# Optimization experiments

Measured on AMD Instinct MI355X. Metric: run time of the kernel, lower is better.

The kernel has to match this reference:

```python
import jax, jax.numpy as jnp
import numpy as np

EMBED = 50
SEQ = 100
NLABEL = 15
HID = 20
VOCAB = 50000
BATCH = 8192


def gru_scan(xs, W, U, b, return_sequences):
    """Keras GRUCell (reset_after=True, gate order z,r,h).
    xs: (B, T, D). W: (D, 3H), U: (H, 3H), b: (2, 3H) [input bias, recurrent bias].
    """
    B = xs.shape[0]
    H = U.shape[0]
    bi, br = b[0], b[1]
    h0 = jnp.zeros((B, H), dtype=xs.dtype)

    def step(h, x_t):
        mx = x_t @ W + bi                      # (B, 3H)
        mh = h @ U + br                        # (B, 3H)
        xz, xr, xh = mx[:, :H], mx[:, H:2*H], mx[:, 2*H:]
        hz, hr, hh_ = mh[:, :H], mh[:, H:2*H], mh[:, 2*H:]
        z = jax.nn.sigmoid(xz + hz)
        r = jax.nn.sigmoid(xr + hr)
        hh = jnp.tanh(xh + r * hh_)
        h_new = z * h + (1.0 - z) * hh
        return h_new, h_new

    xs_t = jnp.swapaxes(xs, 0, 1)              # (T, B, D)
    h_last, hs = jax.lax.scan(step, h0, xs_t)
    if return_sequences:
        return jnp.swapaxes(hs, 0, 1)          # (B, T, H)
    return h_last                               # (B, H)


def setup_inputs() -> dict:
    key = jax.random.key(0)
    ks = jax.random.split(key, 9)
    s = 0.05
    return {
        "x": jax.random.randint(ks[0], (BATCH, SEQ), 0, VOCAB),
        "emb_table": jax.random.normal(ks[1], (VOCAB, EMBED), jnp.float32) * s,
        "W1": jax.random.normal(ks[2], (EMBED, 3 * HID), jnp.float32) * s,
        "U1": jax.random.normal(ks[3], (HID, 3 * HID), jnp.float32) * s,
        "b1": jnp.zeros((2, 3 * HID), jnp.float32),
        "W2": jax.random.normal(ks[4], (HID, 3 * HID), jnp.float32) * s,
        "U2": jax.random.normal(ks[5], (HID, 3 * HID), jnp.float32) * s,
        "b2": jnp.zeros((2, 3 * HID), jnp.float32),
        "Wd": jax.random.normal(ks[6], (HID, NLABEL), jnp.float32) * s,
        "bd": jnp.zeros((NLABEL,), jnp.float32),
        "drop_rate": 0,
    }


def reference(x, emb_table, W1, U1, b1, W2, U2, b2, Wd, bd, drop_rate):
    emb = emb_table[x]                               # (B, T, E)
    seq = gru_scan(emb, W1, U1, b1, return_sequences=True)   # (B, T, H)
    enc = gru_scan(seq, W2, U2, b2, return_sequences=False)  # (B, H)
    # drop_rate == 0 -> tf.nn.dropout is identity
    logits = enc @ Wd + bd                           # (B, 15)
    return logits
```

## Files before the change

kernel.cpp:

```cpp
#include <hip/hip_runtime.h>
#include <hip/hip_bf16.h>
#include <hip/hip_fp16.h>

#define SEQ_T 100
#define HID 20
#define EMB_D 50
#define VOCAB_N 50000
#define TABW 60
#define NTILE 3125
#define BBLK 782

typedef short sh8 __attribute__((ext_vector_type(8)));
typedef float f4  __attribute__((ext_vector_type(4)));

#define OFF_U1P 0
#define OFF_W2P 600
#define OFF_U2P 1200
#define OFF_B1  3600
#define OFF_B2  3720
#define OFF_WD  3840
#define OFF_BD  4140
#define OFF_TAB 4160

__device__ __forceinline__ float ldf(const void* p, int i, int isf) {
  return isf ? ((const float*)p)[i]
             : __bfloat162float(((const __hip_bfloat16*)p)[i]);
}
__device__ __forceinline__ short f2bf(float f) {
  unsigned u = __float_as_uint(f);
  u += 0x7fffu + ((u >> 16) & 1u);
  return (short)(u >> 16);
}
__device__ __forceinline__ float rdl(float v, int l) {
  return __uint_as_float(__builtin_amdgcn_readlane(__float_as_uint(v), l));
}
__device__ __forceinline__ int detect_isf(const void* emb) {
  uint4 dv = ((const uint4*)emb)[threadIdx.x & 63];
  int big = 0;
#pragma unroll
  for (int i = 0; i < 4; ++i) {
    unsigned w = ((const unsigned*)&dv)[i];
    big |= (((w >> 7) & 0xFF) >= 140) | (((w >> 23) & 0xFF) >= 140);
  }
  return (__ballot(big) != 0ull) ? 1 : 0;
}

__global__ __launch_bounds__(256) void build_table(
    const void* __restrict__ emb, const void* __restrict__ W1,
    const void* __restrict__ b1,
    const void* __restrict__ U1, const void* __restrict__ W2,
    const void* __restrict__ U2, const void* __restrict__ b2,
    const void* __restrict__ Wd, const void* __restrict__ bd,
    float* __restrict__ ws)
{
  const int isf = detect_isf(emb);
  if (blockIdx.x == 0) {
    const int t = threadIdx.x;
    unsigned* wsu = (unsigned*)ws;
    for (int i = t; i < 600; i += 256) {
      const int j = i / 10, p = i % 10;
      const int k0 = 2 * p, k1 = 2 * p + 1;
#define PK(M) ((unsigned)__half_as_ushort(__float2half_rn(ldf(M, k0 * 60 + j, isf))) | \
               ((unsigned)__half_as_ushort(__float2half_rn(ldf(M, k1 * 60 + j, isf))) << 16))
      wsu[OFF_U1P + i] = PK(U1);
      wsu[OFF_W2P + i] = PK(W2);
      wsu[OFF_U2P + i] = PK(U2);
#undef PK
    }
    for (int i = t; i < 120; i += 256) {
      ws[OFF_B1 + i] = ldf(b1, i, isf);
      ws[OFF_B2 + i] = ldf(b2, i, isf);
    }
    for (int i = t; i < 300; i += 256) ws[OFF_WD + i] = ldf(Wd, i, isf);
    for (int i = t; i < 15;  i += 256) ws[OFF_BD + i] = ldf(bd, i, isf);
  }

  const int L = threadIdx.x & 63, q = L >> 4, c = L & 15;
  const int wid = blockIdx.x * 4 + (threadIdx.x >> 6);
  float* __restrict__ tab = ws + OFF_TAB;

  __shared__ int4 sB[64][8];
  if (threadIdx.x < 64) {
#pragma unroll
    for (int nt = 0; nt < 4; ++nt) {
      const int col = nt * 16 + c;
      sh8 B0, B1;
#pragma unroll
      for (int jj = 0; jj < 8; ++jj) {
        const int k0 = q * 8 + jj, k1 = 32 + q * 8 + jj;
        B0[jj] = (col < TABW) ? f2bf(ldf(W1, k0 * TABW + col, isf)) : (short)0;
        B1[jj] = (col < TABW && k1 < EMB_D)
                     ? f2bf(ldf(W1, k1 * TABW + col, isf)) : (short)0;
      }
      sB[L][nt * 2]     = *(const int4*)&B0;
      sB[L][nt * 2 + 1] = *(const int4*)&B1;
    }
  }
  float bi[4];
#pragma unroll
  for (int nt = 0; nt < 4; ++nt) {
    const int col = nt * 16 + c;
    bi[nt] = (col < TABW) ? ldf(b1, col, isf) : 0.f;
  }
  __syncthreads();

  for (int tile = wid; tile < NTILE; tile += BBLK * 4) {
    const int v0 = tile * 16;
    sh8 A0, A1;
#pragma unroll
    for (int jj = 0; jj < 8; ++jj) { A0[jj] = 0; A1[jj] = 0; }
    if (!isf) {
      const unsigned short* eb = (const unsigned short*)emb;
      const size_t rb = (size_t)(v0 + c) * EMB_D;
#pragma unroll
      for (int i = 0; i < 4; ++i) {
        unsigned d = *(const unsigned*)(eb + rb + q * 8 + 2 * i);
        A0[2 * i] = (short)(d & 0xffff); A0[2 * i + 1] = (short)(d >> 16);
      }
      const int k1b = 32 + q * 8;
#pragma unroll
      for (int i = 0; i < 4; ++i) {
        const int k = k1b + 2 * i;
        if (k + 1 < EMB_D) {
          unsigned d = *(const unsigned*)(eb + rb + k);
          A1[2 * i] = (short)(d & 0xffff); A1[2 * i + 1] = (short)(d >> 16);
        }
      }
    } else {
      const float* ef = (const float*)emb;
      const size_t rb = (size_t)(v0 + c) * EMB_D;
#pragma unroll
      for (int jj = 0; jj < 8; ++jj) {
        const int k0 = q * 8 + jj, k1 = 32 + q * 8 + jj;
        A0[jj] = f2bf(ef[rb + k0]);
        A1[jj] = (k1 < EMB_D) ? f2bf(ef[rb + k1]) : (short)0;
      }
    }
#pragma unroll
    for (int nt = 0; nt < 4; ++nt) {
      int4 b0i = sB[L][nt * 2], b1i = sB[L][nt * 2 + 1];
      sh8 B0 = *(const sh8*)&b0i, B1 = *(const sh8*)&b1i;
      const int col = nt * 16 + c;
      f4 acc = { bi[nt], bi[nt], bi[nt], bi[nt] };
      acc = __builtin_amdgcn_mfma_f32_16x16x32_bf16(A0, B0, acc, 0, 0, 0);
      acc = __builtin_amdgcn_mfma_f32_16x16x32_bf16(A1, B1, acc, 0, 0, 0);
      if (col < TABW) {
#pragma unroll
        for (int r = 0; r < 4; ++r)
          tab[(size_t)(v0 + q * 4 + r) * TABW + col] = acc[r];
      }
    }
  }
}

__global__ __launch_bounds__(256, 8) void gru_main(
    const int* __restrict__ x, const float* __restrict__ ws,
    const void* __restrict__ emb, void* __restrict__ out)
{
  const int isf = detect_isf(emb);
  const int j = threadIdx.x & 63;
  const int e = __builtin_amdgcn_readfirstlane(blockIdx.x * 4 + (threadIdx.x >> 6));
  const int jc = j < TABW ? j : 0;

  const int* xr = x + (size_t)e * SEQ_T;
  const float* tab = ws + OFF_TAB;
  const int o1 = jc * 40;
  const int jc4 = jc * 4;
  const int a1 = ((j - 20) & 63) * 4;
  const int a2 = ((j + 40) & 63) * 4;
  const float br1 = ws[OFF_B1 + 60 + jc];
  const float bi2 = ws[OFF_B2 + jc];
  const float br2 = ws[OFF_B2 + 60 + jc];
  float h2out;

  asm volatile(
    "global_load_dwordx4 v[10:13], %[o1], %[wsp] offset:0\n\t"
    "global_load_dwordx4 v[14:17], %[o1], %[wsp] offset:16\n\t"
    "global_load_dwordx2 v[18:19], %[o1], %[wsp] offset:32\n\t"
    "v_add_u32 v44, 0x960, %[o1]\n\t"
    "v_add_u32 v45, 0x12c0, %[o1]\n\t"
    "global_load_dwordx4 v[20:23], v44, %[wsp] offset:0\n\t"
    "global_load_dwordx4 v[24:27], v44, %[wsp] offset:16\n\t"
    "global_load_dwordx2 v[28:29], v44, %[wsp] offset:32\n\t"
    "global_load_dwordx4 v[30:33], v45, %[wsp] offset:0\n\t"
    "global_load_dwordx4 v[34:37], v45, %[wsp] offset:16\n\t"
    "global_load_dwordx2 v[38:39], v45, %[wsp] offset:32\n\t"
    "s_mov_b64 s[20:21], 0\n\ts_mov_b64 s[22:23], 0\n\t"
    "s_mov_b64 s[24:25], 0\n\ts_mov_b64 s[26:27], 0\n\t"
    "s_mov_b64 s[28:29], 0\n\t"
    "s_mov_b64 s[30:31], 0\n\ts_mov_b64 s[32:33], 0\n\t"
    "s_mov_b64 s[34:35], 0\n\ts_mov_b64 s[36:37], 0\n\t"
    "s_mov_b64 s[38:39], 0\n\t"
    "v_mov_b32 v40, 0\n\t"
    "v_mov_b32 v41, 0\n\t"
    "s_load_dword s65, %[xp], 0x0\n\t"
    "s_load_dword s66, %[xp], 0x4\n\t"
    "s_waitcnt lgkmcnt(0)\n\t"
    "s_mul_i32 s65, s65, 240\n\t"
    "s_mul_i32 s66, s66, 240\n\t"
    "v_add_u32 v50, s65, %[jc4]\n\t"
    "global_load_dword v42, v50, %[tabp]\n\t"
    "v_add_u32 v50, s66, %[jc4]\n\t"
    "global_load_dword v43, v50, %[tabp]\n\t"
    "s_load_dword s65, %[xp], 0x8\n\t"
    "s_movk_i32 s64, 0xc\n\t"
    "s_movk_i32 s67, 0x64\n\t"
    "s_waitcnt vmcnt(0)\n\t"
    "0:\n\t"
    "v_mov_b32 v44, %[br1]\n\t"
    "v_dot2_f32_f16 v44, s20, v10, v44\n\t"
    "v_dot2_f32_f16 v44, s21, v11, v44\n\t"
    "v_dot2_f32_f16 v44, s22, v12, v44\n\t"
    "v_dot2_f32_f16 v44, s23, v13, v44\n\t"
    "v_dot2_f32_f16 v44, s24, v14, v44\n\t"
    "v_dot2_f32_f16 v44, s25, v15, v44\n\t"
    "v_dot2_f32_f16 v44, s26, v16, v44\n\t"
    "v_dot2_f32_f16 v44, s27, v17, v44\n\t"
    "v_dot2_f32_f16 v44, s28, v18, v44\n\t"
    "v_dot2_f32_f16 v44, s29, v19, v44\n\t"
    "v_add_f32 v45, v42, v44\n\t"
    "v_mul_f32 v45, 0xbfb8aa3b, v45\n\t"
    "v_exp_f32 v45, v45\n\t"
    "s_nop 1\n\t"
    "v_add_f32 v45, 1.0, v45\n\t"
    "v_rcp_f32 v45, v45\n\t"
    "s_nop 1\n\t"
    "ds_bpermute_b32 v46, %[a1], v45\n\t"
    "s_waitcnt lgkmcnt(0)\n\t"
    "v_fma_f32 v47, v46, v44, v42\n\t"
    "v_mul_f32 v47, 0x4038aa3b, v47\n\t"
    "v_exp_f32 v47, v47\n\t"
    "s_nop 1\n\t"
    "v_add_f32 v47, 1.0, v47\n\t"
    "v_rcp_f32 v47, v47\n\t"
    "s_nop 1\n\t"
    "v_fma_f32 v47, -2.0, v47, 1.0\n\t"
    "ds_bpermute_b32 v46, %[a2], v47\n\t"
    "s_waitcnt lgkmcnt(0)\n\t"
    "v_sub_f32 v48, v40, v46\n\t"
    "v_fma_f32 v40, v45, v48, v46\n\t"
    "s_nop 1\n\t"
    "v_cvt_f16_f32 v46, v40\n\t"
    "s_nop 1\n\t"
    "ds_swizzle_b32 v47, v46 offset:0x041F\n\t"
    "s_waitcnt lgkmcnt(0)\n\t"
    "v_pack_b32_f16 v46, v46, v47\n\t"
    "s_nop 1\n\t"
    "v_readlane_b32 s20, v46, 0\n\t"
    "v_readlane_b32 s21, v46, 2\n\t"
    "v_readlane_b32 s22, v46, 4\n\t"
    "v_readlane_b32 s23, v46, 6\n\t"
    "v_readlane_b32 s24, v46, 8\n\t"
    "v_readlane_b32 s25, v46, 10\n\t"
    "v_readlane_b32 s26, v46, 12\n\t"
    "v_readlane_b32 s27, v46, 14\n\t"
    "v_readlane_b32 s28, v46, 16\n\t"
    "v_readlane_b32 s29, v46, 18\n\t"
    "s_mul_i32 s66, s65, 240\n\t"
    "v_add_u32 v50, s66, %[jc4]\n\t"
    "s_waitcnt vmcnt(0)\n\t"
    "v_mov_b32 v42, v43\n\t"
    "global_load_dword v43, v50, %[tabp]\n\t"
    "s_min_u32 s64, s64, 396\n\t"
    "s_load_dword s65, %[xp], s64\n\t"
    "s_add_u32 s64, s64, 4\n\t"
    "v_mov_b32 v44, %[bi2]\n\t"
    "v_mov_b32 v48, %[br2]\n\t"
    "v_dot2_f32_f16 v44, s20, v20, v44\n\t"
    "v_dot2_f32_f16 v48, s30, v30, v48\n\t"
    "v_dot2_f32_f16 v44, s21, v21, v44\n\t"
    "v_dot2_f32_f16 v48, s31, v31, v48\n\t"
    "v_dot2_f32_f16 v44, s22, v22, v44\n\t"
    "v_dot2_f32_f16 v48, s32, v32, v48\n\t"
    "v_dot2_f32_f16 v44, s23, v23, v44\n\t"
    "v_dot2_f32_f16 v48, s33, v33, v48\n\t"
    "v_dot2_f32_f16 v44, s24, v24, v44\n\t"
    "v_dot2_f32_f16 v48, s34, v34, v48\n\t"
    "v_dot2_f32_f16 v44, s25, v25, v44\n\t"
    "v_dot2_f32_f16 v48, s35, v35, v48\n\t"
    "v_dot2_f32_f16 v44, s26, v26, v44\n\t"
    "v_dot2_f32_f16 v48, s36, v36, v48\n\t"
    "v_dot2_f32_f16 v44, s27, v27, v44\n\t"
    "v_dot2_f32_f16 v48, s37, v37, v48\n\t"
    "v_dot2_f32_f16 v44, s28, v28, v44\n\t"
    "v_dot2_f32_f16 v48, s38, v38, v48\n\t"
    "v_dot2_f32_f16 v44, s29, v29, v44\n\t"
    "v_dot2_f32_f16 v48, s39, v39, v48\n\t"
    "v_add_f32 v45, v44, v48\n\t"
    "v_mul_f32 v45, 0xbfb8aa3b, v45\n\t"
    "v_exp_f32 v45, v45\n\t"
    "s_nop 1\n\t"
    "v_add_f32 v45, 1.0, v45\n\t"
    "v_rcp_f32 v45, v45\n\t"
    "s_nop 1\n\t"
    "ds_bpermute_b32 v46, %[a1], v45\n\t"
    "s_waitcnt lgkmcnt(0)\n\t"
    "v_fma_f32 v47, v46, v48, v44\n\t"
    "v_mul_f32 v47, 0x4038aa3b, v47\n\t"
    "v_exp_f32 v47, v47\n\t"
    "s_nop 1\n\t"
    "v_add_f32 v47, 1.0, v47\n\t"
    "v_rcp_f32 v47, v47\n\t"
    "s_nop 1\n\t"
    "v_fma_f32 v47, -2.0, v47, 1.0\n\t"
    "ds_bpermute_b32 v46, %[a2], v47\n\t"
    "s_waitcnt lgkmcnt(0)\n\t"
    "v_sub_f32 v49, v41, v46\n\t"
    "v_fma_f32 v41, v45, v49, v46\n\t"
    "s_nop 1\n\t"
    "v_cvt_f16_f32 v46, v41\n\t"
    "s_nop 1\n\t"
    "ds_swizzle_b32 v47, v46 offset:0x041F\n\t"
    "s_waitcnt lgkmcnt(0)\n\t"
    "v_pack_b32_f16 v46, v46, v47\n\t"
    "s_nop 1\n\t"
    "v_readlane_b32 s30, v46, 0\n\t"
    "v_readlane_b32 s31, v46, 2\n\t"
    "v_readlane_b32 s32, v46, 4\n\t"
    "v_readlane_b32 s33, v46, 6\n\t"
    "v_readlane_b32 s34, v46, 8\n\t"
    "v_readlane_b32 s35, v46, 10\n\t"
    "v_readlane_b32 s36, v46, 12\n\t"
    "v_readlane_b32 s37, v46, 14\n\t"
    "v_readlane_b32 s38, v46, 16\n\t"
    "v_readlane_b32 s39, v46, 18\n\t"
    "s_sub_u32 s67, s67, 1\n\t"
    "s_cmp_lg_u32 s67, 0\n\t"
    "s_cbranch_scc1 0b\n\t"
    "s_waitcnt vmcnt(0) lgkmcnt(0)\n\t"
    "v_mov_b32 %[h2o], v41\n\t"
    : [h2o] "=v"(h2out)
    : [wsp] "s"(ws), [xp] "s"(xr), [tabp] "s"(tab),
      [o1] "v"(o1), [jc4] "v"(jc4), [a1] "v"(a1), [a2] "v"(a2),
      [br1] "v"(br1), [bi2] "v"(bi2), [br2] "v"(br2)
    : "memory", "vcc", "scc",
      "v10","v11","v12","v13","v14","v15","v16","v17","v18","v19",
      "v20","v21","v22","v23","v24","v25","v26","v27","v28","v29",
      "v30","v31","v32","v33","v34","v35","v36","v37","v38","v39",
      "v40","v41","v42","v43","v44","v45","v46","v47","v48","v49","v50",
      "s20","s21","s22","s23","s24","s25","s26","s27","s28","s29",
      "s30","s31","s32","s33","s34","s35","s36","s37","s38","s39",
      "s64","s65","s66","s67");

  if (j < 15) {
    float a = ws[OFF_BD + j];
#pragma unroll
    for (int k = 0; k < HID; ++k)
      a = fmaf(rdl(h2out, k), ws[OFF_WD + k * 15 + j], a);
    if (isf) ((float*)out)[(size_t)e * 15 + j] = a;
    else ((__hip_bfloat16*)out)[(size_t)e * 15 + j] = __float2bfloat16(a);
  }
}

extern "C" void kernel_launch(void* const* d_in, const int* in_sizes, int n_in,
                              void* d_out, int out_size, void* d_ws, size_t ws_size,
                              hipStream_t stream) {
  const int* x    = (const int*)d_in[0];
  const void* emb = d_in[1];
  const void* W1  = d_in[2];
  const void* U1  = d_in[3];
  const void* b1  = d_in[4];
  const void* W2  = d_in[5];
  const void* U2  = d_in[6];
  const void* b2  = d_in[7];
  const void* Wd  = d_in[8];
  const void* bd  = d_in[9];
  float* ws = (float*)d_ws;

  build_table<<<BBLK, 256, 0, stream>>>(
      emb, W1, b1, U1, W2, U2, b2, Wd, bd, ws);
  gru_main<<<2048, 256, 0, stream>>>(x, ws, emb, d_out);
}
```

Before: 240.6 us.

## Interleave two batch rows per wave, wavefront-skew GRU layers, fold exp scales into weights

Each wave now processes two sequences interleaved, so their independent dependency chains can hide each other's latency. Layer 1 and layer 2 are skewed by one timestep and computed in the same iteration. The hidden state is passed through LDS ds_write/ds_read instead of readlane into SGPRs. The log2e sigmoid/tanh scaling constants are folded into the packed weights, biases and the precomputed input table. The table is stored as fp16 instead of fp32 to halve gather traffic. The costs are a much higher VGPR footprint (occupancy hint lowered to 4), half as many blocks, and extra fp16 rounding of the table.

```diff
diff --git a/kernel.cpp b/kernel.cpp
--- a/kernel.cpp
+++ b/kernel.cpp
@@ -43,6 +43,9 @@
     big |= (((w >> 7) & 0xFF) >= 140) | (((w >> 23) & 0xFF) >= 140);
   }
   return (__ballot(big) != 0ull) ? 1 : 0;
+}
+__device__ __forceinline__ float gsc(int col) {
+  return (col < 40) ? -1.44269504f : 2.88539008f;
 }
 
 __global__ __launch_bounds__(256) void build_table(
@@ -60,16 +63,17 @@
     for (int i = t; i < 600; i += 256) {
       const int j = i / 10, p = i % 10;
       const int k0 = 2 * p, k1 = 2 * p + 1;
-#define PK(M) ((unsigned)__half_as_ushort(__float2half_rn(ldf(M, k0 * 60 + j, isf))) | \
-               ((unsigned)__half_as_ushort(__float2half_rn(ldf(M, k1 * 60 + j, isf))) << 16))
+      const float s = gsc(j);
+#define PK(M) ((unsigned)__half_as_ushort(__float2half_rn(ldf(M, k0 * 60 + j, isf) * s)) | \
+               ((unsigned)__half_as_ushort(__float2half_rn(ldf(M, k1 * 60 + j, isf) * s)) << 16))
       wsu[OFF_U1P + i] = PK(U1);
       wsu[OFF_W2P + i] = PK(W2);
       wsu[OFF_U2P + i] = PK(U2);
 #undef PK
     }
     for (int i = t; i < 120; i += 256) {
-      ws[OFF_B1 + i] = ldf(b1, i, isf);
-      ws[OFF_B2 + i] = ldf(b2, i, isf);
+      ws[OFF_B1 + i] = ldf(b1, i, isf) * (i >= 60 ? gsc(i - 60) : 1.f);
+      ws[OFF_B2 + i] = ldf(b2, i, isf) * gsc(i % 60);
     }
     for (int i = t; i < 300; i += 256) ws[OFF_WD + i] = ldf(Wd, i, isf);
     for (int i = t; i < 15;  i += 256) ws[OFF_BD + i] = ldf(bd, i, isf);
@@ -77,7 +81,7 @@
 
   const int L = threadIdx.x & 63, q = L >> 4, c = L & 15;
   const int wid = blockIdx.x * 4 + (threadIdx.x >> 6);
-  float* __restrict__ tab = ws + OFF_TAB;
+  unsigned short* __restrict__ tab16 = (unsigned short*)(ws + OFF_TAB);
 
   __shared__ int4 sB[64][8];
   if (threadIdx.x < 64) {
@@ -145,210 +149,491 @@
       acc = __builtin_amdgcn_mfma_f32_16x16x32_bf16(A0, B0, acc, 0, 0, 0);
       acc = __builtin_amdgcn_mfma_f32_16x16x32_bf16(A1, B1, acc, 0, 0, 0);
       if (col < TABW) {
+        const float s = gsc(col);
 #pragma unroll
         for (int r = 0; r < 4; ++r)
-          tab[(size_t)(v0 + q * 4 + r) * TABW + col] = acc[r];
+          tab16[(size_t)(v0 + q * 4 + r) * TABW + col] =
+              __half_as_ushort(__float2half_rn(acc[r] * s));
       }
     }
   }
 }
 
-__global__ __launch_bounds__(256, 8) void gru_main(
+__global__ __launch_bounds__(256, 4) void gru_main(
     const int* __restrict__ x, const float* __restrict__ ws,
     const void* __restrict__ emb, void* __restrict__ out)
 {
   const int isf = detect_isf(emb);
   const int j = threadIdx.x & 63;
-  const int e = __builtin_amdgcn_readfirstlane(blockIdx.x * 4 + (threadIdx.x >> 6));
+  const int e = __builtin_amdgcn_readfirstlane(blockIdx.x * 8 + (threadIdx.x >> 6) * 2);
   const int jc = j < TABW ? j : 0;
 
   const int* xr = x + (size_t)e * SEQ_T;
-  const float* tab = ws + OFF_TAB;
+  const unsigned short* tab = (const unsigned short*)(ws + OFF_TAB);
   const int o1 = jc * 40;
-  const int jc4 = jc * 4;
+  const int jc2 = jc * 2;
   const int a1 = ((j - 20) & 63) * 4;
   const int a2 = ((j + 40) & 63) * 4;
   const float br1 = ws[OFF_B1 + 60 + jc];
   const float bi2 = ws[OFF_B2 + jc];
   const float br2 = ws[OFF_B2 + 60 + jc];
-  float h2out;
+
+  __shared__ char sbuf[2048];
+  const unsigned lb = (unsigned)(uintptr_t)&sbuf[0] + (threadIdx.x >> 6) * 512;
+  const int lmap = (j < 20 ? 2 * j : 40 + 2 * (j - 20));
+  const int wadA = (int)(lb + lmap),       radA = (int)lb;
+  const int wadB = (int)(lb + 256 + lmap), radB = (int)(lb + 256);
+  float h2oA, h2oB;
 
   asm volatile(
     "global_load_dwordx4 v[10:13], %[o1], %[wsp] offset:0\n\t"
     "global_load_dwordx4 v[14:17], %[o1], %[wsp] offset:16\n\t"
     "global_load_dwordx2 v[18:19], %[o1], %[wsp] offset:32\n\t"
-    "v_add_u32 v44, 0x960, %[o1]\n\t"
-    "v_add_u32 v45, 0x12c0, %[o1]\n\t"
-    "global_load_dwordx4 v[20:23], v44, %[wsp] offset:0\n\t"
-    "global_load_dwordx4 v[24:27], v44, %[wsp] offset:16\n\t"
-    "global_load_dwordx2 v[28:29], v44, %[wsp] offset:32\n\t"
-    "global_load_dwordx4 v[30:33], v45, %[wsp] offset:0\n\t"
-    "global_load_dwordx4 v[34:37], v45, %[wsp] offset:16\n\t"
-    "global_load_dwordx2 v[38:39], v45, %[wsp] offset:32\n\t"
-    "s_mov_b64 s[20:21], 0\n\ts_mov_b64 s[22:23], 0\n\t"
-    "s_mov_b64 s[24:25], 0\n\ts_mov_b64 s[26:27], 0\n\t"
-    "s_mov_b64 s[28:29], 0\n\t"
-    "s_mov_b64 s[30:31], 0\n\ts_mov_b64 s[32:33], 0\n\t"
-    "s_mov_b64 s[34:35], 0\n\ts_mov_b64 s[36:37], 0\n\t"
-    "s_mov_b64 s[38:39], 0\n\t"
-    "v_mov_b32 v40, 0\n\t"
-    "v_mov_b32 v41, 0\n\t"
+    "v_add_u32 v98, 0x960, %[o1]\n\t"
+    "v_add_u32 v109, 0x12c0, %[o1]\n\t"
+    "global_load_dwordx4 v[20:23], v98, %[wsp] offset:0\n\t"
+    "global_load_dwordx4 v[24:27], v98, %[wsp] offset:16\n\t"
+    "global_load_dwordx2 v[28:29], v98, %[wsp] offset:32\n\t"
+    "global_load_dwordx4 v[30:33], v109, %[wsp] offset:0\n\t"
+    "global_load_dwordx4 v[34:37], v109, %[wsp] offset:16\n\t"
+    "global_load_dwordx2 v[38:39], v109, %[wsp] offset:32\n\t"
+    "v_mov_b32 v80, 0\n\tv_mov_b32 v81, 0\n\t"
+    "v_mov_b32 v82, 0\n\tv_mov_b32 v83, 0\n\t"
+    "v_mov_b32 v50, 0\n\tv_mov_b32 v51, 0\n\t"
+    "v_mov_b32 v52, 0\n\tv_mov_b32 v53, 0\n\t"
+    "v_mov_b32 v54, 0\n\tv_mov_b32 v55, 0\n\t"
+    "v_mov_b32 v56, 0\n\tv_mov_b32 v57, 0\n\t"
+    "v_mov_b32 v58, 0\n\tv_mov_b32 v59, 0\n\t"
+    "v_mov_b32 v70, 0\n\tv_mov_b32 v71, 0\n\t"
+    "v_mov_b32 v72, 0\n\tv_mov_b32 v73, 0\n\t"
+    "v_mov_b32 v74, 0\n\tv_mov_b32 v75, 0\n\t"
+    "v_mov_b32 v76, 0\n\tv_mov_b32 v77, 0\n\t"
+    "v_mov_b32 v78, 0\n\tv_mov_b32 v79, 0\n\t"
     "s_load_dword s65, %[xp], 0x0\n\t"
     "s_load_dword s66, %[xp], 0x4\n\t"
-    "s_waitcnt lgkmcnt(0)\n\t"
-    "s_mul_i32 s65, s65, 240\n\t"
-    "s_mul_i32 s66, s66, 240\n\t"
-    "v_add_u32 v50, s65, %[jc4]\n\t"
-    "global_load_dword v42, v50, %[tabp]\n\t"
-    "v_add_u32 v50, s66, %[jc4]\n\t"
-    "global_load_dword v43, v50, %[tabp]\n\t"
-    "s_load_dword s65, %[xp], 0x8\n\t"
-    "s_movk_i32 s64, 0xc\n\t"
-    "s_movk_i32 s67, 0x64\n\t"
-    "s_waitcnt vmcnt(0)\n\t"
+    "s_load_dword s68, %[xp], 0x8\n\t"
+    "s_load_dword s71, %[xp], 0x190\n\t"
+    "s_load_dword s72, %[xp], 0x194\n\t"
+    "s_load_dword s73, %[xp], 0x198\n\t"
+    "s_waitcnt lgkmcnt(0)\n\t"
+    "s_mul_i32 s65, s65, 120\n\t"
+    "s_mul_i32 s66, s66, 120\n\t"
+    "s_mul_i32 s68, s68, 120\n\t"
+    "s_mul_i32 s71, s71, 120\n\t"
+    "s_mul_i32 s72, s72, 120\n\t"
+    "s_mul_i32 s73, s73, 120\n\t"
+    "v_add_u32 v98, s65, %[jc2]\n\t"
+    "global_load_ushort v97, v98, %[tabp]\n\t"
+    "v_add_u32 v98, s71, %[jc2]\n\t"
+    "global_load_ushort v108, v98, %[tabp]\n\t"
+    "v_add_u32 v98, s66, %[jc2]\n\t"
+    "global_load_ushort v84, v98, %[tabp]\n\t"
+    "v_add_u32 v98, s72, %[jc2]\n\t"
+    "global_load_ushort v86, v98, %[tabp]\n\t"
+    "v_add_u32 v98, s68, %[jc2]\n\t"
+    "global_load_ushort v85, v98, %[tabp]\n\t"
+    "v_add_u32 v98, s73, %[jc2]\n\t"
+    "global_load_ushort v87, v98, %[tabp]\n\t"
+    "s_load_dword s65, %[xp], 0xc\n\t"
+    "s_load_dword s68, %[xp], 0x10\n\t"
+    "s_load_dword s71, %[xp], 0x19c\n\t"
+    "s_load_dword s73, %[xp], 0x1a0\n\t"
+    "s_movk_i32 s64, 0x14\n\t"
+    "s_movk_i32 s69, 0x18\n\t"
+    "s_movk_i32 s70, 0x1a4\n\t"
+    "s_movk_i32 s72, 0x1a8\n\t"
+    "s_movk_i32 s67, 0x32\n\t"
+    "s_waitcnt vmcnt(4)\n\t"
+    "v_cvt_f32_f16 v97, v97\n\t"
+    "v_cvt_f32_f16 v108, v108\n\t"
+    "v_mov_b32 v88, %[br1]\n\t"
+    "v_mov_b32 v99, %[br1]\n\t"
+    "v_add_f32 v91, v97, v88\n\t"
+    "v_add_f32 v102, v108, v99\n\t"
+    "v_exp_f32 v91, v91\n\t"
+    "v_exp_f32 v102, v102\n\t"
+    "s_nop 1\n\t"
+    "v_add_f32 v91, 1.0, v91\n\t"
+    "v_add_f32 v102, 1.0, v102\n\t"
+    "v_rcp_f32 v91, v91\n\t"
+    "v_rcp_f32 v102, v102\n\t"
+    "s_nop 1\n\t"
+    "ds_bpermute_b32 v93, %[a1], v91\n\t"
+    "ds_bpermute_b32 v104, %[a1], v102\n\t"
+    "s_waitcnt lgkmcnt(0)\n\t"
+    "v_fma_f32 v95, v93, v88, v97\n\t"
+    "v_fma_f32 v106, v104, v99, v108\n\t"
+    "v_exp_f32 v95, v95\n\t"
+    "v_exp_f32 v106, v106\n\t"
+    "s_nop 1\n\t"
+    "v_add_f32 v95, 1.0, v95\n\t"
+    "v_add_f32 v106, 1.0, v106\n\t"
+    "v_rcp_f32 v95, v95\n\t"
+    "v_rcp_f32 v106, v106\n\t"
+    "s_nop 1\n\t"
+    "v_fma_f32 v95, -2.0, v95, 1.0\n\t"
+    "v_fma_f32 v106, -2.0, v106, 1.0\n\t"
+    "ds_bpermute_b32 v93, %[a2], v95\n\t"
+    "ds_bpermute_b32 v104, %[a2], v106\n\t"
+    "s_waitcnt lgkmcnt(0)\n\t"
+    "v_sub_f32 v97, v80, v93\n\t"
+    "v_fma_f32 v80, v91, v97, v93\n\t"
+    "v_sub_f32 v108, v82, v104\n\t"
+    "v_fma_f32 v82, v102, v108, v104\n\t"
+    "v_cvt_f16_f32 v93, v80\n\t"
+    "v_cvt_f16_f32 v104, v82\n\t"
+    "s_nop 1\n\t"
+    "ds_write_b16 %[wadA], v93\n\t"
+    "ds_write_b16 %[wadB], v104\n\t"
+    "ds_read_b128 v[40:43], %[radA]\n\t"
+    "ds_read_b128 v[44:47], %[radA] offset:16\n\t"
+    "ds_read_b64  v[48:49], %[radA] offset:32\n\t"
+    "ds_read_b128 v[60:63], %[radB]\n\t"
+    "ds_read_b128 v[64:67], %[radB] offset:16\n\t"
+    "ds_read_b64  v[68:69], %[radB] offset:32\n\t"
     "0:\n\t"
-    "v_mov_b32 v44, %[br1]\n\t"
-    "v_dot2_f32_f16 v44, s20, v10, v44\n\t"
-    "v_dot2_f32_f16 v44, s21, v11, v44\n\t"
-    "v_dot2_f32_f16 v44, s22, v12, v44\n\t"
-    "v_dot2_f32_f16 v44, s23, v13, v44\n\t"
-    "v_dot2_f32_f16 v44, s24, v14, v44\n\t"
-    "v_dot2_f32_f16 v44, s25, v15, v44\n\t"
-    "v_dot2_f32_f16 v44, s26, v16, v44\n\t"
-    "v_dot2_f32_f16 v44, s27, v17, v44\n\t"
-    "v_dot2_f32_f16 v44, s28, v18, v44\n\t"
-    "v_dot2_f32_f16 v44, s29, v19, v44\n\t"
-    "v_add_f32 v45, v42, v44\n\t"
-    "v_mul_f32 v45, 0xbfb8aa3b, v45\n\t"
-    "v_exp_f32 v45, v45\n\t"
+    "s_waitcnt lgkmcnt(0)\n\t"
+    "v_dot2_f32_f16 v88, v40, v10, %[br1]\n\t"
+    "v_dot2_f32_f16 v89, v40, v20, %[bi2]\n\t"
+    "v_dot2_f32_f16 v90, v50, v30, %[br2]\n\t"
+    "v_dot2_f32_f16 v99, v60, v10, %[br1]\n\t"
+    "v_dot2_f32_f16 v100, v60, v20, %[bi2]\n\t"
+    "v_dot2_f32_f16 v101, v70, v30, %[br2]\n\t"
+    "v_dot2_f32_f16 v88, v41, v11, v88\n\t"
+    "v_dot2_f32_f16 v89, v41, v21, v89\n\t"
+    "v_dot2_f32_f16 v90, v51, v31, v90\n\t"
+    "v_dot2_f32_f16 v99, v61, v11, v99\n\t"
+    "v_dot2_f32_f16 v100, v61, v21, v100\n\t"
+    "v_dot2_f32_f16 v101, v71, v31, v101\n\t"
+    "v_dot2_f32_f16 v88, v42, v12, v88\n\t"
+    "v_dot2_f32_f16 v89, v42, v22, v89\n\t"
+    "v_dot2_f32_f16 v90, v52, v32, v90\n\t"
+    "v_dot2_f32_f16 v99, v62, v12, v99\n\t"
+    "v_dot2_f32_f16 v100, v62, v22, v100\n\t"
+    "v_dot2_f32_f16 v101, v72, v32, v101\n\t"
+    "v_dot2_f32_f16 v88, v43, v13, v88\n\t"
+    "v_dot2_f32_f16 v89, v43, v23, v89\n\t"
+    "v_dot2_f32_f16 v90, v53, v33, v90\n\t"
+    "v_dot2_f32_f16 v99, v63, v13, v99\n\t"
+    "v_dot2_f32_f16 v100, v63, v23, v100\n\t"
+    "v_dot2_f32_f16 v101, v73, v33, v101\n\t"
+    "v_dot2_f32_f16 v88, v44, v14, v88\n\t"
+    "v_dot2_f32_f16 v89, v44, v24, v89\n\t"
+    "v_dot2_f32_f16 v90, v54, v34, v90\n\t"
+    "v_dot2_f32_f16 v99, v64, v14, v99\n\t"
+    "v_dot2_f32_f16 v100, v64, v24, v100\n\t"
+    "v_dot2_f32_f16 v101, v74, v34, v101\n\t"
+    "v_dot2_f32_f16 v88, v45, v15, v88\n\t"
+    "v_dot2_f32_f16 v89, v45, v25, v89\n\t"
+    "v_dot2_f32_f16 v90, v55, v35, v90\n\t"
+    "v_dot2_f32_f16 v99, v65, v15, v99\n\t"
+    "v_dot2_f32_f16 v100, v65, v25, v100\n\t"
+    "v_dot2_f32_f16 v101, v75, v35, v101\n\t"
+    "v_dot2_f32_f16 v88, v46, v16, v88\n\t"
+    "v_dot2_f32_f16 v89, v46, v26, v89\n\t"
+    "v_dot2_f32_f16 v90, v56, v36, v90\n\t"
+    "v_dot2_f32_f16 v99, v66, v16, v99\n\t"
+    "v_dot2_f32_f16 v100, v66, v26, v100\n\t"
+    "v_dot2_f32_f16 v101, v76, v36, v101\n\t"
+    "v_dot2_f32_f16 v88, v47, v17, v88\n\t"
+    "v_dot2_f32_f16 v89, v47, v27, v89\n\t"
+    "v_dot2_f32_f16 v90, v57, v37, v90\n\t"
+    "v_dot2_f32_f16 v99, v67, v17, v99\n\t"
+    "v_dot2_f32_f16 v100, v67, v27, v100\n\t"
+    "v_dot2_f32_f16 v101, v77, v37, v101\n\t"
+    "v_dot2_f32_f16 v88, v48, v18, v88\n\t"
+    "v_dot2_f32_f16 v89, v48, v28, v89\n\t"
+    "v_dot2_f32_f16 v90, v58, v38, v90\n\t"
+    "v_dot2_f32_f16 v99, v68, v18, v99\n\t"
+    "v_dot2_f32_f16 v100, v68, v28, v100\n\t"
+    "v_dot2_f32_f16 v101, v78, v38, v101\n\t"
+    "v_dot2_f32_f16 v88, v49, v19, v88\n\t"
+    "v_dot2_f32_f16 v89, v49, v29, v89\n\t"
+    "v_dot2_f32_f16 v90, v59, v39, v90\n\t"
+    "v_dot2_f32_f16 v99, v69, v19, v99\n\t"
+    "v_dot2_f32_f16 v100, v69, v29, v100\n\t"
+    "v_dot2_f32_f16 v101, v79, v39, v101\n\t"
+    "s_waitcnt vmcnt(2)\n\t"
+    "v_cvt_f32_f16 v84, v84\n\t"
+    "v_cvt_f32_f16 v86, v86\n\t"
     "s_nop 1\n\t"
-    "v_add_f32 v45, 1.0, v45\n\t"
-    "v_rcp_f32 v45, v45\n\t"
+    "v_add_f32 v91, v84, v88\n\t"
+    "v_add_f32 v92, v89, v90\n\t"
+    "v_add_f32 v102, v86, v99\n\t"
+    "v_add_f32 v103, v100, v101\n\t"
+    "v_exp_f32 v91, v91\n\t"
+    "v_exp_f32 v92, v92\n\t"
+    "v_exp_f32 v102, v102\n\t"
+    "v_exp_f32 v103, v103\n\t"
+    "v_add_f32 v91, 1.0, v91\n\t"
+    "v_add_f32 v92, 1.0, v92\n\t"
+    "v_add_f32 v102, 1.0, v102\n\t"
+    "v_add_f32 v103, 1.0, v103\n\t"
+    "v_rcp_f32 v91, v91\n\t"
+    "v_rcp_f32 v92, v92\n\t"
+    "v_rcp_f32 v102, v102\n\t"
+    "v_rcp_f32 v103, v103\n\t"
+    "ds_bpermute_b32 v93, %[a1], v91\n\t"
+    "ds_bpermute_b32 v94, %[a1], v92\n\t"
+    "ds_bpermute_b32 v104, %[a1], v102\n\t"
+    "ds_bpermute_b32 v105, %[a1], v103\n\t"
+    "s_waitcnt lgkmcnt(0)\n\t"
+    "v_fma_f32 v95, v93, v88, v84\n\t"
+    "v_fma_f32 v96, v94, v90, v89\n\t"
+    "v_fma_f32 v106, v104, v99, v86\n\t"
+    "v_fma_f32 v107, v105, v101, v100\n\t"
+    "s_mul_i32 s66, s65, 120\n\t"
+    "v_add_u32 v98, s66, %[jc2]\n\t"
+    "global_load_ushort v84, v98, %[tabp]\n\t"
+    "s_min_u32 s64, s64, 0x18c\n\t"
+    "s_load_dword s65, %[xp], s64\n\t"
+    "s_add_u32 s64, s64, 8\n\t"
+    "s_mul_i32 s66, s71, 120\n\t"
+    "v_add_u32 v109, s66, %[jc2]\n\t"
+    "global_load_ushort v86, v109, %[tabp]\n\t"
+    "s_min_u32 s70, s70, 0x31c\n\t"
+    "s_load_dword s71, %[xp], s70\n\t"
+    "s_add_u32 s70, s70, 8\n\t"
+    "v_exp_f32 v95, v95\n\t"
+    "v_exp_f32 v96, v96\n\t"
+    "v_exp_f32 v106, v106\n\t"
+    "v_exp_f32 v107, v107\n\t"
+    "v_add_f32 v95, 1.0, v95\n\t"
+    "v_add_f32 v96, 1.0, v96\n\t"
+    "v_add_f32 v106, 1.0, v106\n\t"
+    "v_add_f32 v107, 1.0, v107\n\t"
+    "v_rcp_f32 v95, v95\n\t"
+    "v_rcp_f32 v96, v96\n\t"
+    "v_rcp_f32 v106, v106\n\t"
+    "v_rcp_f32 v107, v107\n\t"
+    "v_fma_f32 v95, -2.0, v95, 1.0\n\t"
+    "v_fma_f32 v96, -2.0, v96, 1.0\n\t"
+    "v_fma_f32 v106, -2.0, v106, 1.0\n\t"
+    "v_fma_f32 v107, -2.0, v107, 1.0\n\t"
+    "ds_bpermute_b32 v93, %[a2], v95\n\t"
+    "ds_bpermute_b32 v94, %[a2], v96\n\t"
+    "ds_bpermute_b32 v104, %[a2], v106\n\t"
+    "ds_bpermute_b32 v105, %[a2], v107\n\t"
+    "s_waitcnt lgkmcnt(0)\n\t"
+    "v_sub_f32 v97, v80, v93\n\t"
+    "v_fma_f32 v80, v91, v97, v93\n\t"
+    "v_sub_f32 v97, v81, v94\n\t"
+    "v_fma_f32 v81, v92, v97, v94\n\t"
+    "v_sub_f32 v108, v82, v104\n\t"
+    "v_fma_f32 v82, v102, v108, v104\n\t"
+    "v_sub_f32 v108, v83, v105\n\t"
+    "v_fma_f32 v83, v103, v108, v105\n\t"
+    "v_cvt_f16_f32 v93, v80\n\t"
+    "v_cvt_f16_f32 v94, v81\n\t"
+    "v_cvt_f16_f32 v104, v82\n\t"
+    "v_cvt_f16_f32 v105, v83\n\t"
+    "ds_write_b16 %[wadA], v93\n\t"
+    "ds_write_b16 %[wadA], v94 offset:128\n\t"
+    "ds_write_b16 %[wadB], v104\n\t"
+    "ds_write_b16 %[wadB], v105 offset:128\n\t"
+    "ds_read_b128 v[40:43], %[radA]\n\t"
+    "ds_read_b128 v[44:47], %[radA] offset:16\n\t"
+    "ds_read_b64  v[48:49], %[radA] offset:32\n\t"
+    "ds_read_b128 v[50:53], %[radA] offset:128\n\t"
+    "ds_read_b128 v[54:57], %[radA] offset:144\n\t"
+    "ds_read_b64  v[58:59], %[radA] offset:160\n\t"
+    "ds_read_b128 v[60:63], %[radB]\n\t"
+    "ds_read_b128 v[64:67], %[radB] offset:16\n\t"
+    "ds_read_b64  v[68:69], %[radB] offset:32\n\t"
+    "ds_read_b128 v[70:73], %[radB] offset:128\n\t"
+    "ds_read_b128 v[74:77], %[radB] offset:144\n\t"
+    "ds_read_b64  v[78:79], %[radB] offset:160\n\t"
+    "s_waitcnt lgkmcnt(0)\n\t"
+    "v_dot2_f32_f16 v88, v40, v10, %[br1]\n\t"
+    "v_dot2_f32_f16 v89, v40, v20, %[bi2]\n\t"
+    "v_dot2_f32_f16 v90, v50, v30, %[br2]\n\t"
+    "v_dot2_f32_f16 v99, v60, v10, %[br1]\n\t"
+    "v_dot2_f32_f16 v100, v60, v20, %[bi2]\n\t"
+    "v_dot2_f32_f16 v101, v70, v30, %[br2]\n\t"
+    "v_dot2_f32_f16 v88, v41, v11, v88\n\t"
+    "v_dot2_f32_f16 v89, v41, v21, v89\n\t"
+    "v_dot2_f32_f16 v90, v51, v31, v90\n\t"
+    "v_dot2_f32_f16 v99, v61, v11, v99\n\t"
+    "v_dot2_f32_f16 v100, v61, v21, v100\n\t"
+    "v_dot2_f32_f16 v101, v71, v31, v101\n\t"
+    "v_dot2_f32_f16 v88, v42, v12, v88\n\t"
+    "v_dot2_f32_f16 v89, v42, v22, v89\n\t"
+    "v_dot2_f32_f16 v90, v52, v32, v90\n\t"
+    "v_dot2_f32_f16 v99, v62, v12, v99\n\t"
+    "v_dot2_f32_f16 v100, v62, v22, v100\n\t"
+    "v_dot2_f32_f16 v101, v72, v32, v101\n\t"
+    "v_dot2_f32_f16 v88, v43, v13, v88\n\t"
+    "v_dot2_f32_f16 v89, v43, v23, v89\n\t"
+    "v_dot2_f32_f16 v90, v53, v33, v90\n\t"
+    "v_dot2_f32_f16 v99, v63, v13, v99\n\t"
+    "v_dot2_f32_f16 v100, v63, v23, v100\n\t"
+    "v_dot2_f32_f16 v101, v73, v33, v101\n\t"
+    "v_dot2_f32_f16 v88, v44, v14, v88\n\t"
+    "v_dot2_f32_f16 v89, v44, v24, v89\n\t"
+    "v_dot2_f32_f16 v90, v54, v34, v90\n\t"
+    "v_dot2_f32_f16 v99, v64, v14, v99\n\t"
+    "v_dot2_f32_f16 v100, v64, v24, v100\n\t"
+    "v_dot2_f32_f16 v101, v74, v34, v101\n\t"
+    "v_dot2_f32_f16 v88, v45, v15, v88\n\t"
+    "v_dot2_f32_f16 v89, v45, v25, v89\n\t"
+    "v_dot2_f32_f16 v90, v55, v35, v90\n\t"
+    "v_dot2_f32_f16 v99, v65, v15, v99\n\t"
+    "v_dot2_f32_f16 v100, v65, v25, v100\n\t"
+    "v_dot2_f32_f16 v101, v75, v35, v101\n\t"
+    "v_dot2_f32_f16 v88, v46, v16, v88\n\t"
+    "v_dot2_f32_f16 v89, v46, v26, v89\n\t"
+    "v_dot2_f32_f16 v90, v56, v36, v90\n\t"
+    "v_dot2_f32_f16 v99, v66, v16, v99\n\t"
+    "v_dot2_f32_f16 v100, v66, v26, v100\n\t"
+    "v_dot2_f32_f16 v101, v76, v36, v101\n\t"
+    "v_dot2_f32_f16 v88, v47, v17, v88\n\t"
+    "v_dot2_f32_f16 v89, v47, v27, v89\n\t"
+    "v_dot2_f32_f16 v90, v57, v37, v90\n\t"
+    "v_dot2_f32_f16 v99, v67, v17, v99\n\t"
+    "v_dot2_f32_f16 v100, v67, v27, v100\n\t"
+    "v_dot2_f32_f16 v101, v77, v37, v101\n\t"
+    "v_dot2_f32_f16 v88, v48, v18, v88\n\t"
+    "v_dot2_f32_f16 v89, v48, v28, v89\n\t"
+    "v_dot2_f32_f16 v90, v58, v38, v90\n\t"
+    "v_dot2_f32_f16 v99, v68, v18, v99\n\t"
+    "v_dot2_f32_f16 v100, v68, v28, v100\n\t"
+    "v_dot2_f32_f16 v101, v78, v38, v101\n\t"
+    "v_dot2_f32_f16 v88, v49, v19, v88\n\t"
+    "v_dot2_f32_f16 v89, v49, v29, v89\n\t"
+    "v_dot2_f32_f16 v90, v59, v39, v90\n\t"
+    "v_dot2_f32_f16 v99, v69, v19, v99\n\t"
+    "v_dot2_f32_f16 v100, v69, v29, v100\n\t"
+    "v_dot2_f32_f16 v101, v79, v39, v101\n\t"
+    "s_waitcnt vmcnt(2)\n\t"
+    "v_cvt_f32_f16 v85, v85\n\t"
+    "v_cvt_f32_f16 v87, v87\n\t"
     "s_nop 1\n\t"
-    "ds_bpermute_b32 v46, %[a1], v45\n\t"
-    "s_waitcnt lgkmcnt(0)\n\t"
-    "v_fma_f32 v47, v46, v44, v42\n\t"
-    "v_mul_f32 v47, 0x4038aa3b, v47\n\t"
-    "v_exp_f32 v47, v47\n\t"
-    "s_nop 1\n\t"
-    "v_add_f32 v47, 1.0, v47\n\t"
-    "v_rcp_f32 v47, v47\n\t"
-    "s_nop 1\n\t"
-    "v_fma_f32 v47, -2.0, v47, 1.0\n\t"
-    "ds_bpermute_b32 v46, %[a2], v47\n\t"
-    "s_waitcnt lgkmcnt(0)\n\t"
-    "v_sub_f32 v48, v40, v46\n\t"
-    "v_fma_f32 v40, v45, v48, v46\n\t"
-    "s_nop 1\n\t"
-    "v_cvt_f16_f32 v46, v40\n\t"
-    "s_nop 1\n\t"
-    "ds_swizzle_b32 v47, v46 offset:0x041F\n\t"
-    "s_waitcnt lgkmcnt(0)\n\t"
-    "v_pack_b32_f16 v46, v46, v47\n\t"
-    "s_nop 1\n\t"
-    "v_readlane_b32 s20, v46, 0\n\t"
-    "v_readlane_b32 s21, v46, 2\n\t"
-    "v_readlane_b32 s22, v46, 4\n\t"
-    "v_readlane_b32 s23, v46, 6\n\t"
-    "v_readlane_b32 s24, v46, 8\n\t"
-    "v_readlane_b32 s25, v46, 10\n\t"
-    "v_readlane_b32 s26, v46, 12\n\t"
-    "v_readlane_b32 s27, v46, 14\n\t"
-    "v_readlane_b32 s28, v46, 16\n\t"
-    "v_readlane_b32 s29, v46, 18\n\t"
-    "s_mul_i32 s66, s65, 240\n\t"
-    "v_add_u32 v50, s66, %[jc4]\n\t"
-    "s_waitcnt vmcnt(0)\n\t"
-    "v_mov_b32 v42, v43\n\t"
-    "global_load_dword v43, v50, %[tabp]\n\t"
-    "s_min_u32 s64, s64, 396\n\t"
-    "s_load_dword s65, %[xp], s64\n\t"
-    "s_add_u32 s64, s64, 4\n\t"
-    "v_mov_b32 v44, %[bi2]\n\t"
-    "v_mov_b32 v48, %[br2]\n\t"
-    "v_dot2_f32_f16 v44, s20, v20, v44\n\t"
-    "v_dot2_f32_f16 v48, s30, v30, v48\n\t"
-    "v_dot2_f32_f16 v44, s21, v21, v44\n\t"
-    "v_dot2_f32_f16 v48, s31, v31, v48\n\t"
-    "v_dot2_f32_f16 v44, s22, v22, v44\n\t"
-    "v_dot2_f32_f16 v48, s32, v32, v48\n\t"
-    "v_dot2_f32_f16 v44, s23, v23, v44\n\t"
-    "v_dot2_f32_f16 v48, s33, v33, v48\n\t"
-    "v_dot2_f32_f16 v44, s24, v24, v44\n\t"
-    "v_dot2_f32_f16 v48, s34, v34, v48\n\t"
-    "v_dot2_f32_f16 v44, s25, v25, v44\n\t"
-    "v_dot2_f32_f16 v48, s35, v35, v48\n\t"
-    "v_dot2_f32_f16 v44, s26, v26, v44\n\t"
-    "v_dot2_f32_f16 v48, s36, v36, v48\n\t"
-    "v_dot2_f32_f16 v44, s27, v27, v44\n\t"
-    "v_dot2_f32_f16 v48, s37, v37, v48\n\t"
-    "v_dot2_f32_f16 v44, s28, v28, v44\n\t"
-    "v_dot2_f32_f16 v48, s38, v38, v48\n\t"
-    "v_dot2_f32_f16 v44, s29, v29, v44\n\t"
-    "v_dot2_f32_f16 v48, s39, v39, v48\n\t"
-    "v_add_f32 v45, v44, v48\n\t"
-    "v_mul_f32 v45, 0xbfb8aa3b, v45\n\t"
-    "v_exp_f32 v45, v45\n\t"
-    "s_nop 1\n\t"
-    "v_add_f32 v45, 1.0, v45\n\t"
-    "v_rcp_f32 v45, v45\n\t"
-    "s_nop 1\n\t"
-    "ds_bpermute_b32 v46, %[a1], v45\n\t"
-    "s_waitcnt lgkmcnt(0)\n\t"
-    "v_fma_f32 v47, v46, v48, v44\n\t"
-    "v_mul_f32 v47, 0x4038aa3b, v47\n\t"
-    "v_exp_f32 v47, v47\n\t"
-    "s_nop 1\n\t"
-    "v_add_f32 v47, 1.0, v47\n\t"
-    "v_rcp_f32 v47, v47\n\t"
-    "s_nop 1\n\t"
-    "v_fma_f32 v47, -2.0, v47, 1.0\n\t"
-    "ds_bpermute_b32 v46, %[a2], v47\n\t"
-    "s_waitcnt lgkmcnt(0)\n\t"
-    "v_sub_f32 v49, v41, v46\n\t"
-    "v_fma_f32 v41, v45, v49, v46\n\t"
-    "s_nop 1\n\t"
-    "v_cvt_f16_f32 v46, v41\n\t"
-    "s_nop 1\n\t"
-    "ds_swizzle_b32 v47, v46 offset:0x041F\n\t"
-    "s_waitcnt lgkmcnt(0)\n\t"
-    "v_pack_b32_f16 v46, v46, v47\n\t"
-    "s_nop 1\n\t"
-    "v_readlane_b32 s30, v46, 0\n\t"
-    "v_readlane_b32 s31, v46, 2\n\t"
-    "v_readlane_b32 s32, v46, 4\n\t"
-    "v_readlane_b32 s33, v46, 6\n\t"
-    "v_readlane_b32 s34, v46, 8\n\t"
-    "v_readlane_b32 s35, v46, 10\n\t"
-    "v_readlane_b32 s36, v46, 12\n\t"
-    "v_readlane_b32 s37, v46, 14\n\t"
-    "v_readlane_b32 s38, v46, 16\n\t"
-    "v_readlane_b32 s39, v46, 18\n\t"
+    "v_add_f32 v91, v85, v88\n\t"
+    "v_add_f32 v92, v89, v90\n\t"
+    "v_add_f32 v102, v87, v99\n\t"
+    "v_add_f32 v103, v100, v101\n\t"
+    "v_exp_f32 v91, v91\n\t"
+    "v_exp_f32 v92, v92\n\t"
+    "v_exp_f32 v102, v102\n\t"
+    "v_exp_f32 v103, v103\n\t"
+    "v_add_f32 v91, 1.0, v91\n\t"
+    "v_add_f32 v92, 1.0, v92\n\t"
+    "v_add_f32 v102, 1.0, v102\n\t"
+    "v_add_f32 v103, 1.0, v103\n\t"
+    "v_rcp_f32 v91, v91\n\t"
+    "v_rcp_f32 v92, v92\n\t"
+    "v_rcp_f32 v102, v102\n\t"
+    "v_rcp_f32 v103, v103\n\t"
+    "ds_bpermute_b32 v93, %[a1], v91\n\t"
+    "ds_bpermute_b32 v94, %[a1], v92\n\t"
+    "ds_bpermute_b32 v104, %[a1], v102\n\t"
+    "ds_bpermute_b32 v105, %[a1], v103\n\t"
+    "s_waitcnt lgkmcnt(0)\n\t"
+    "v_fma_f32 v95, v93, v88, v85\n\t"
+    "v_fma_f32 v96, v94, v90, v89\n\t"
+    "v_fma_f32 v106, v104, v99, v87\n\t"
+    "v_fma_f32 v107, v105, v101, v100\n\t"
+    "s_mul_i32 s66, s68, 120\n\t"
+    "v_add_u32 v98, s66, %[jc2]\n\t"
+    "global_load_ushort v85, v98, %[tabp]\n\t"
+    "s_min_u32 s69, s69, 0x188\n\t"
+    "s_load_dword s68, %[xp], s69\n\t"
+    "s_add_u32 s69, s69, 8\n\t"
+    "s_mul_i32 s66, s73, 120\n\t"
+    "v_add_u32 v109, s66, %[jc2]\n\t"
+    "global_load_ushort v87, v109, %[tabp]\n\t"
+    "s_min_u32 s72, s72, 0x318\n\t"
+    "s_load_dword s73, %[xp], s72\n\t"
+    "s_add_u32 s72, s72, 8\n\t"
+    "v_exp_f32 v95, v95\n\t"
+    "v_exp_f32 v96, v96\n\t"
+    "v_exp_f32 v106, v106\n\t"
+    "v_exp_f32 v107, v107\n\t"
+    "v_add_f32 v95, 1.0, v95\n\t"
+    "v_add_f32 v96, 1.0, v96\n\t"
+    "v_add_f32 v106, 1.0, v106\n\t"
+    "v_add_f32 v107, 1.0, v107\n\t"
+    "v_rcp_f32 v95, v95\n\t"
+    "v_rcp_f32 v96, v96\n\t"
+    "v_rcp_f32 v106, v106\n\t"
+    "v_rcp_f32 v107, v107\n\t"
+    "v_fma_f32 v95, -2.0, v95, 1.0\n\t"
+    "v_fma_f32 v96, -2.0, v96, 1.0\n\t"
+    "v_fma_f32 v106, -2.0, v106, 1.0\n\t"
+    "v_fma_f32 v107, -2.0, v107, 1.0\n\t"
+    "ds_bpermute_b32 v93, %[a2], v95\n\t"
+    "ds_bpermute_b32 v94, %[a2], v96\n\t"
+    "ds_bpermute_b32 v104, %[a2], v106\n\t"
+    "ds_bpermute_b32 v105, %[a2], v107\n\t"
+    "s_waitcnt lgkmcnt(0)\n\t"
+    "v_sub_f32 v97, v80, v93\n\t"
+    "v_fma_f32 v80, v91, v97, v93\n\t"
+    "v_sub_f32 v97, v81, v94\n\t"
+    "v_fma_f32 v81, v92, v97, v94\n\t"
+    "v_sub_f32 v108, v82, v104\n\t"
+    "v_fma_f32 v82, v102, v108, v104\n\t"
+    "v_sub_f32 v108, v83, v105\n\t"
+    "v_fma_f32 v83, v103, v108, v105\n\t"
+    "v_cvt_f16_f32 v93, v80\n\t"
+    "v_cvt_f16_f32 v94, v81\n\t"
+    "v_cvt_f16_f32 v104, v82\n\t"
+    "v_cvt_f16_f32 v105, v83\n\t"
+    "ds_write_b16 %[wadA], v93\n\t"
+    "ds_write_b16 %[wadA], v94 offset:128\n\t"
+    "ds_write_b16 %[wadB], v104\n\t"
+    "ds_write_b16 %[wadB], v105 offset:128\n\t"
+    "ds_read_b128 v[40:43], %[radA]\n\t"
+    "ds_read_b128 v[44:47], %[radA] offset:16\n\t"
+    "ds_read_b64  v[48:49], %[radA] offset:32\n\t"
+    "ds_read_b128 v[50:53], %[radA] offset:128\n\t"
+    "ds_read_b128 v[54:57], %[radA] offset:144\n\t"
+    "ds_read_b64  v[58:59], %[radA] offset:160\n\t"
+    "ds_read_b128 v[60:63], %[radB]\n\t"
+    "ds_read_b128 v[64:67], %[radB] offset:16\n\t"
+    "ds_read_b64  v[68:69], %[radB] offset:32\n\t"
+    "ds_read_b128 v[70:73], %[radB] offset:128\n\t"
+    "ds_read_b128 v[74:77], %[radB] offset:144\n\t"
+    "ds_read_b64  v[78:79], %[radB] offset:160\n\t"
     "s_sub_u32 s67, s67, 1\n\t"
     "s_cmp_lg_u32 s67, 0\n\t"
     "s_cbranch_scc1 0b\n\t"
     "s_waitcnt vmcnt(0) lgkmcnt(0)\n\t"
-    "v_mov_b32 %[h2o], v41\n\t"
-    : [h2o] "=v"(h2out)
+    "v_mov_b32 %[hA], v81\n\t"
+    "v_mov_b32 %[hB], v83\n\t"
+    : [hA] "=v"(h2oA), [hB] "=v"(h2oB)
     : [wsp] "s"(ws), [xp] "s"(xr), [tabp] "s"(tab),
-      [o1] "v"(o1), [jc4] "v"(jc4), [a1] "v"(a1), [a2] "v"(a2),
-      [br1] "v"(br1), [bi2] "v"(bi2), [br2] "v"(br2)
+      [o1] "v"(o1), [jc2] "v"(jc2), [a1] "v"(a1), [a2] "v"(a2),
+      [br1] "v"(br1), [bi2] "v"(bi2), [br2] "v"(br2),
+      [wadA] "v"(wadA), [radA] "v"(radA), [wadB] "v"(wadB), [radB] "v"(radB)
     : "memory", "vcc", "scc",
       "v10","v11","v12","v13","v14","v15","v16","v17","v18","v19",
       "v20","v21","v22","v23","v24","v25","v26","v27","v28","v29",
       "v30","v31","v32","v33","v34","v35","v36","v37","v38","v39",
-      "v40","v41","v42","v43","v44","v45","v46","v47","v48","v49","v50",
-      "s20","s21","s22","s23","s24","s25","s26","s27","s28","s29",
-      "s30","s31","s32","s33","s34","s35","s36","s37","s38","s39",
-      "s64","s65","s66","s67");
+      "v40","v41","v42","v43","v44","v45","v46","v47","v48","v49",
+      "v50","v51","v52","v53","v54","v55","v56","v57","v58","v59",
+      "v60","v61","v62","v63","v64","v65","v66","v67","v68","v69",
+      "v70","v71","v72","v73","v74","v75","v76","v77","v78","v79",
+      "v80","v81","v82","v83","v84","v85","v86","v87","v88","v89",
+      "v90","v91","v92","v93","v94","v95","v96","v97","v98","v99",
+      "v100","v101","v102","v103","v104","v105","v106","v107","v108","v109",
+      "s64","s65","s66","s67","s68","s69","s70","s71","s72","s73");
 
   if (j < 15) {
     float a = ws[OFF_BD + j];
-#pragma unroll
-    for (int k = 0; k < HID; ++k)
-      a = fmaf(rdl(h2out, k), ws[OFF_WD + k * 15 + j], a);
-    if (isf) ((float*)out)[(size_t)e * 15 + j] = a;
-    else ((__hip_bfloat16*)out)[(size_t)e * 15 + j] = __float2bfloat16(a);
+    float b = a;
+#pragma unroll
+    for (int k = 0; k < HID; ++k) {
+      const float w = ws[OFF_WD + k * 15 + j];
+      a = fmaf(rdl(h2oA, k), w, a);
+      b = fmaf(rdl(h2oB, k), w, b);
+    }
+    if (isf) {
+      ((float*)out)[(size_t)e * 15 + j] = a;
+      ((float*)out)[(size_t)(e + 1) * 15 + j] = b;
+    } else {
+      ((__hip_bfloat16*)out)[(size_t)e * 15 + j] = __float2bfloat16(a);
+      ((__hip_bfloat16*)out)[(size_t)(e + 1) * 15 + j] = __float2bfloat16(b);
+    }
   }
 }
 
@@ -369,5 +654,5 @@
 
   build_table<<<BBLK, 256, 0, stream>>>(
       emb, W1, b1, U1, W2, U2, b2, Wd, bd, ws);
-  gru_main<<<2048, 256, 0, stream>>>(x, ws, emb, d_out);
-}
+  gru_main<<<1024, 256, 0, stream>>>(x, ws, emb, d_out);
+}
```

Measured after the change: 204.7 us. 14.9% less time.
